# Optimization experiments

Measured on AMD Instinct MI355X. Metric: run time of the kernel, lower is better.

Reference implementation:

```python
import jax, jax.numpy as jnp
import numpy as np

B, T, K = 32, 8192, 16
EPS = 1e-7
LAM_FIRE, LAM_CANCEL, LAM_VALID, LAM_WRITE = 1.0, 1.0, 0.5, 0.5


def setup_inputs() -> dict:
    key = jax.random.key(0)
    ks = jax.random.split(key, 11)
    return {
        "trigger_hazard": jax.random.uniform(ks[0], (B, T, K), jnp.float32),
        "validity": jax.random.uniform(ks[1], (B, T, K), jnp.float32),
        "cancel_logits": jax.random.normal(ks[2], (B, T, K, 3), jnp.float32),
        "write_score": jax.random.normal(ks[3], (B, T, 1), jnp.float32),
        "live_mask": jax.random.randint(ks[4], (B, T, K), 0, 2).astype(bool),
        "contract_id": jax.random.randint(ks[5], (B, T, K), 0, 32),
        "oracle_fire": jax.random.randint(ks[6], (B, T, K), 0, 2).astype(jnp.float32),
        "oracle_cancel": jax.random.randint(ks[7], (B, T, K), 0, 4),
        "oracle_valid": jax.random.randint(ks[8], (B, T, K), 0, 2).astype(jnp.float32),
        "oracle_should_write": jax.random.randint(ks[9], (B, T, 1), 0, 2).astype(jnp.float32),
        "oracle_contract_id": jax.random.randint(ks[10], (B, T, K), 0, 32),
    }


def _masked_bce(p_raw, y, m):
    # Mirrors torch: BCE(clamp(p)*mask, y*mask), then *mask, sum / clamp(mask.sum(),1)
    n = jnp.maximum(m.sum(), 1.0)
    p = jnp.clip(p_raw, EPS, 1.0 - EPS) * m
    t = y * m
    # extra inner clip only guards masked entries (p==0), which are zeroed anyway
    bce = -(t * jnp.log(jnp.clip(p, EPS)) + (1.0 - t) * jnp.log(jnp.clip(1.0 - p, EPS)))
    return (bce * m).sum() / n


def _cancel_ce(logits, cancel_tgt, live_mask):
    has = ((cancel_tgt > 0) & live_mask).astype(jnp.float32)  # (B,T,K)
    n = has.sum()
    tgt = jnp.clip(cancel_tgt - 1, 0).astype(jnp.int32)
    logp = jax.nn.log_softmax(logits, axis=-1)  # (B,T,K,3)
    ce = -jnp.take_along_axis(logp, tgt[..., None], axis=-1)[..., 0]
    return jnp.where(n > 0, (ce * has).sum() / jnp.maximum(n, 1.0), 0.0)


def _bce_with_logits(x, y):
    return jnp.mean(jnp.maximum(x, 0.0) - x * y + jnp.log1p(jnp.exp(-jnp.abs(x))))


def reference(trigger_hazard, validity, cancel_logits, write_score, live_mask,
              contract_id, oracle_fire, oracle_cancel, oracle_valid,
              oracle_should_write, oracle_contract_id):
    # Vectorized align_oracle_to_model: broadcast compare + first-match argmax + gather
    match = (contract_id[..., :, None] == oracle_contract_id[..., None, :]) \
            & (contract_id != 0)[..., None]              # (B,T,Km,Ko)
    found = match.any(axis=-1)                           # (B,T,Km)
    idx = jnp.argmax(match, axis=-1)                     # first matching oracle slot

    def align_f(x):  # float tensors -> zeros where unmatched (torch out = zeros float)
        return jnp.where(found, jnp.take_along_axis(x, idx, axis=2), 0.0)

    fire_t = align_f(oracle_fire)
    valid_t = align_f(oracle_valid)
    cancel_t = jnp.where(found, jnp.take_along_axis(oracle_cancel, idx, axis=2), 0)

    m = live_mask.astype(jnp.float32)
    fire = LAM_FIRE * _masked_bce(trigger_hazard, fire_t, m)
    cancel = LAM_CANCEL * _cancel_ce(cancel_logits, cancel_t, live_mask)
    valid = LAM_VALID * _masked_bce(validity, valid_t, m)
    write = LAM_WRITE * _bce_with_logits(write_score, oracle_should_write)
    total = fire + cancel + valid + write
    return jnp.stack([fire, cancel, valid, write, total])
```

## Files before the change

kernel.cpp:

```cpp
#include <hip/hip_runtime.h>
#include <math.h>

#define EPS_F 1e-7f

constexpr int Bc = 32, Tc = 8192, Kc = 16;
constexpr int ROWS   = Bc * Tc;
constexpr int BLOCK  = 256;
constexpr int NITEM4 = ROWS * 4;
constexpr int NBLK   = NITEM4 / BLOCK;
constexpr int ROWS_PER_BLK = BLOCK / 4;

constexpr int R_OCID = 0 * 4096;
constexpr int R_OCAN = 1 * 4096;
constexpr int R_OFIR = 2 * 4096;
constexpr int R_OVAL = 3 * 4096;
constexpr int R_CID  = 4 * 4096;
constexpr int R_LIVE = 5 * 4096;
constexpr int R_TRIG = 6 * 4096;
constexpr int R_VALP = 7 * 4096;
constexpr int R_CLOG = 8 * 4096;
constexpr int R_WSC  = R_CLOG + 12288;
constexpr int R_OSW  = R_WSC + 256;
constexpr int SMEM_BYTES = R_OSW + 256;

typedef unsigned long long u64;

__device__ __forceinline__ u64 shflx64(u64 v, int m) {
  unsigned lo = __shfl_xor((unsigned)v, m, 64);
  unsigned hi = __shfl_xor((unsigned)(v >> 32), m, 64);
  return ((u64)hi << 32) | lo;
}

__device__ __forceinline__ void dma16(void* lds, const void* g) {
  __builtin_amdgcn_global_load_lds(
      (const __attribute__((address_space(1))) void*)g,
      (__attribute__((address_space(3))) void*)lds, 16, 0, 0);
}
__device__ __forceinline__ void dma4(void* lds, const void* g) {
  __builtin_amdgcn_global_load_lds(
      (const __attribute__((address_space(1))) void*)g,
      (__attribute__((address_space(3))) void*)lds, 4, 0, 0);
}

__global__ __launch_bounds__(BLOCK) void loss_main(
    const float* __restrict__ trig,
    const float* __restrict__ valp,
    const float* __restrict__ clog,
    const float* __restrict__ wscore,
    const int*   __restrict__ live,
    const int*   __restrict__ cid,
    const float* __restrict__ ofire,
    const int*   __restrict__ ocan,
    const float* __restrict__ ovalid,
    const float* __restrict__ oshw,
    const int*   __restrict__ ocid,
    float* __restrict__ part)
{
  __shared__ __align__(16) char smem[SMEM_BYTES];

  const int tid  = threadIdx.x;
  const int lane = tid & 63;
  const int w    = tid >> 6;
  const int t0   = blockIdx.x * BLOCK;
  const int gi   = t0 + w * 64 + lane;

  {
    char* sb = smem + w * 1024;
    const size_t o16 = (size_t)gi * 16;
    dma16(sb + R_OCID, (const char*)ocid  + o16);
    dma16(sb + R_OCAN, (const char*)ocan  + o16);
    dma16(sb + R_OFIR, (const char*)ofire + o16);
    dma16(sb + R_OVAL, (const char*)ovalid+ o16);
    dma16(sb + R_CID,  (const char*)cid   + o16);
    dma16(sb + R_LIVE, (const char*)live  + o16);
    dma16(sb + R_TRIG, (const char*)trig  + o16);
    dma16(sb + R_VALP, (const char*)valp  + o16);
    const char* gc = (const char*)clog + (size_t)(t0 + w * 64) * 48;
    char* sc = smem + R_CLOG + w * 3072;
    dma16(sc + 0,    gc + 0    + lane * 16);
    dma16(sc + 1024, gc + 1024 + lane * 16);
    dma16(sc + 2048, gc + 2048 + lane * 16);
    const int r0 = blockIdx.x * ROWS_PER_BLK;
    if (w == 0)      dma4(smem + R_WSC, (const char*)wscore + (size_t)(r0 + lane) * 4);
    else if (w == 1) dma4(smem + R_OSW, (const char*)oshw   + (size_t)(r0 + lane) * 4);
  }
  __syncthreads();

  const int4   oc = *(const int4*)  (smem + R_OCID + tid * 16);
  const int4   cc = *(const int4*)  (smem + R_OCAN + tid * 16);
  const float4 ff = *(const float4*)(smem + R_OFIR + tid * 16);
  const float4 vv = *(const float4*)(smem + R_OVAL + tid * 16);
  const int4   cd = *(const int4*)  (smem + R_CID  + tid * 16);
  const int4   lm = *(const int4*)  (smem + R_LIVE + tid * 16);
  const float4 ph = *(const float4*)(smem + R_TRIG + tid * 16);
  const float4 pq = *(const float4*)(smem + R_VALP + tid * 16);
  const float4 lA = *(const float4*)(smem + R_CLOG + tid * 48 + 0);
  const float4 lB = *(const float4*)(smem + R_CLOG + tid * 48 + 16);
  const float4 lC = *(const float4*)(smem + R_CLOG + tid * 48 + 32);
  const float  wx = *(const float*) (smem + R_WSC + (tid >> 2) * 4);
  const float  wy = *(const float*) (smem + R_OSW + (tid >> 2) * 4);

  u64 tblLo = 0ull, tblHi = 0ull, fndLo = 0ull, fndHi = 0ull;
  {
    const int   ocs[4] = {oc.x, oc.y, oc.z, oc.w};
    const int   ccs[4] = {cc.x, cc.y, cc.z, cc.w};
    const float ffs[4] = {ff.x, ff.y, ff.z, ff.w};
    const float vvs[4] = {vv.x, vv.y, vv.z, vv.w};
    #pragma unroll
    for (int j = 0; j < 4; ++j) {
      const unsigned c  = (unsigned)ocs[j] & 31u;
      const unsigned sh = (c & 15u) * 4u;
      const bool isLo   = c < 16u;
      const bool seen   = (((isLo ? fndLo : fndHi) >> sh) & 1ull) != 0ull;
      const unsigned nib = (unsigned)ffs[j] | ((unsigned)vvs[j] << 1) |
                           ((unsigned)ccs[j] << 2);
      const u64 add  = seen ? 0ull : ((u64)nib << sh);
      const u64 fadd = 0xFull << sh;
      tblLo |= isLo ? add : 0ull;
      tblHi |= isLo ? 0ull : add;
      fndLo |= isLo ? fadd : 0ull;
      fndHi |= isLo ? 0ull : fadd;
    }
  }

  #pragma unroll
  for (int m = 1; m <= 2; m <<= 1) {
    const u64 pTL = shflx64(tblLo, m);
    const u64 pTH = shflx64(tblHi, m);
    const u64 pFL = shflx64(fndLo, m);
    const u64 pFH = shflx64(fndHi, m);
    const bool iLow = (lane & m) == 0;
    const u64 loTL = iLow ? tblLo : pTL, hiTL = iLow ? pTL : tblLo;
    const u64 loTH = iLow ? tblHi : pTH, hiTH = iLow ? pTH : tblHi;
    const u64 loFL = iLow ? fndLo : pFL, hiFL = iLow ? pFL : fndLo;
    const u64 loFH = iLow ? fndHi : pFH, hiFH = iLow ? pFH : fndHi;
    tblLo = loTL | (hiTL & ~loFL);
    tblHi = loTH | (hiTH & ~loFH);
    fndLo = loFL | hiFL;
    fndHi = loFH | hiFH;
  }

  float s0 = 0.f, s1 = 0.f, s2 = 0.f, s3 = 0.f, s4 = 0.f;
  {
    const int   cds[4] = {cd.x, cd.y, cd.z, cd.w};
    const int   lms[4] = {lm.x, lm.y, lm.z, lm.w};
    const float phs[4] = {ph.x, ph.y, ph.z, ph.w};
    const float pqs[4] = {pq.x, pq.y, pq.z, pq.w};
    const float L0[4] = {lA.x, lA.w, lB.z, lC.y};
    const float L1[4] = {lA.y, lB.x, lB.w, lC.z};
    const float L2[4] = {lA.z, lB.y, lC.x, lC.w};
    #pragma unroll
    for (int j = 0; j < 4; ++j) {
      const unsigned c  = (unsigned)cds[j] & 31u;
      const unsigned sh = (c & 15u) * 4u;
      const bool isLo   = c < 16u;
      const bool fnd = (c != 0u) &&
                       ((((isLo ? fndLo : fndHi) >> sh) & 1ull) != 0ull);
      unsigned nib = (unsigned)(((isLo ? tblLo : tblHi) >> sh)) & 15u;
      nib = fnd ? nib : 0u;
      const float fire_t = (float)(nib & 1u);
      const float val_t  = (float)((nib >> 1) & 1u);
      const int   can_t  = (int)(nib >> 2);

      const float m = lms[j] ? 1.f : 0.f;

      const float p  = fminf(fmaxf(phs[j], EPS_F), 1.f - EPS_F);
      const float bf = -__logf((fire_t != 0.f) ? p : 1.f - p);
      const float q  = fminf(fmaxf(pqs[j], EPS_F), 1.f - EPS_F);
      const float bv = -__logf((val_t != 0.f) ? q : 1.f - q);

      const float has = (can_t > 0 && lms[j]) ? 1.f : 0.f;
      const int tgt = (can_t - 1) < 0 ? 0 : (can_t - 1);
      const float l0 = L0[j], l1 = L1[j], l2 = L2[j];
      const float mx  = fmaxf(l0, fmaxf(l1, l2));
      const float lse = mx + __logf(__expf(l0 - mx) + __expf(l1 - mx) +
                                    __expf(l2 - mx));
      const float lt  = (tgt == 0) ? l0 : ((tgt == 1) ? l1 : l2);

      s0 += bf * m;
      s1 += m;
      s2 += (lse - lt) * has;
      s3 += has;
      s4 += bv * m;
    }
  }

  float s5 = 0.f;
  if ((tid & 3) == 0) {
    s5 = fmaxf(wx, 0.f) - wx * wy + __logf(1.f + __expf(-fabsf(wx)));
  }

  float v[6] = {s0, s1, s2, s3, s4, s5};
  #pragma unroll
  for (int off = 32; off > 0; off >>= 1) {
    #pragma unroll
    for (int i = 0; i < 6; ++i) v[i] += __shfl_down(v[i], off, 64);
  }
  __shared__ float red[4][6];
  if (lane == 0) {
    #pragma unroll
    for (int i = 0; i < 6; ++i) red[w][i] = v[i];
  }
  __syncthreads();
  if (tid == 0) {
    #pragma unroll
    for (int i = 0; i < 6; ++i)
      part[blockIdx.x * 6 + i] = red[0][i] + red[1][i] + red[2][i] + red[3][i];
  }
}

__global__ __launch_bounds__(BLOCK) void loss_finalize(
    const float* __restrict__ part, float* __restrict__ out)
{
  double v[6] = {0, 0, 0, 0, 0, 0};
  for (int r = threadIdx.x; r < NBLK; r += BLOCK) {
    #pragma unroll
    for (int i = 0; i < 6; ++i) v[i] += (double)part[r * 6 + i];
  }
  #pragma unroll
  for (int off = 32; off > 0; off >>= 1) {
    #pragma unroll
    for (int i = 0; i < 6; ++i) v[i] += __shfl_down(v[i], off, 64);
  }
  __shared__ double red[4][6];
  const int w = threadIdx.x >> 6, lane = threadIdx.x & 63;
  if (lane == 0) {
    #pragma unroll
    for (int i = 0; i < 6; ++i) red[w][i] = v[i];
  }
  __syncthreads();
  if (threadIdx.x == 0) {
    double a[6];
    #pragma unroll
    for (int i = 0; i < 6; ++i) a[i] = red[0][i] + red[1][i] + red[2][i] + red[3][i];
    const double live_n = a[1] < 1.0 ? 1.0 : a[1];
    const double fire   = a[0] / live_n;
    const double cancel = (a[3] > 0.0) ? a[2] / (a[3] < 1.0 ? 1.0 : a[3])
                                       : 0.0;
    const double valid  = 0.5 * a[4] / live_n;
    const double wr     = 0.5 * a[5] / (double)ROWS;
    out[0] = (float)fire;
    out[1] = (float)cancel;
    out[2] = (float)valid;
    out[3] = (float)wr;
    out[4] = (float)(fire + cancel + valid + wr);
  }
}

extern "C" void kernel_launch(void* const* d_in, const int* in_sizes, int n_in,
                              void* d_out, int out_size, void* d_ws, size_t ws_size,
                              hipStream_t stream) {
  const float* trig   = (const float*)d_in[0];
  const float* valp   = (const float*)d_in[1];
  const float* clog   = (const float*)d_in[2];
  const float* wscore = (const float*)d_in[3];
  const int*   live   = (const int*)  d_in[4];
  const int*   cid    = (const int*)  d_in[5];
  const float* ofire  = (const float*)d_in[6];
  const int*   ocan   = (const int*)  d_in[7];
  const float* ovalid = (const float*)d_in[8];
  const float* oshw   = (const float*)d_in[9];
  const int*   ocid   = (const int*)  d_in[10];
  float* out  = (float*)d_out;
  float* part = (float*)d_ws;

  loss_main<<<NBLK, BLOCK, 0, stream>>>(trig, valp, clog, wscore, live, cid,
                                        ofire, ocan, ovalid, oshw, ocid, part);
  loss_finalize<<<1, BLOCK, 0, stream>>>(part, out);
}
```

Measured before the change: 208.5 us.

## Switch to persistent grid with double-buffered LDS DMA pipeline

Replaces the one-tile-per-block launch with a fixed grid of 768 persistent 128-thread blocks. Each block walks tiles in a grid-stride loop and double-buffers the global-to-LDS DMA loads, using vmcnt waits so the next tile's loads overlap the current tile's compute. This removes per-block launch and tail overhead, and the finalize kernel now reduces far fewer partials. The risks are lower memory-level parallelism per CU, manual waitcnt correctness with no barriers between waves, and clamped tile indices on the last iteration.

```diff
diff --git a/kernel.cpp b/kernel.cpp
--- a/kernel.cpp
+++ b/kernel.cpp
@@ -3,25 +3,28 @@
 
 #define EPS_F 1e-7f
 
-constexpr int Bc = 32, Tc = 8192, Kc = 16;
-constexpr int ROWS   = Bc * Tc;
-constexpr int BLOCK  = 256;
-constexpr int NITEM4 = ROWS * 4;
-constexpr int NBLK   = NITEM4 / BLOCK;
-constexpr int ROWS_PER_BLK = BLOCK / 4;
-
-constexpr int R_OCID = 0 * 4096;
-constexpr int R_OCAN = 1 * 4096;
-constexpr int R_OFIR = 2 * 4096;
-constexpr int R_OVAL = 3 * 4096;
-constexpr int R_CID  = 4 * 4096;
-constexpr int R_LIVE = 5 * 4096;
-constexpr int R_TRIG = 6 * 4096;
-constexpr int R_VALP = 7 * 4096;
-constexpr int R_CLOG = 8 * 4096;
-constexpr int R_WSC  = R_CLOG + 12288;
+constexpr int ROWS  = 32 * 8192;
+constexpr int BLOCK = 128;
+constexpr int TILE_ITEMS = 128;
+constexpr int NT    = (ROWS * 4) / TILE_ITEMS;
+constexpr int GRID  = 768;
+constexpr int KIT   = (NT + GRID - 1) / GRID;
+
+constexpr int R_OCID = 0 * 2048;
+constexpr int R_OCAN = 1 * 2048;
+constexpr int R_OFIR = 2 * 2048;
+constexpr int R_OVAL = 3 * 2048;
+constexpr int R_CID  = 4 * 2048;
+constexpr int R_LIVE = 5 * 2048;
+constexpr int R_TRIG = 6 * 2048;
+constexpr int R_VALP = 7 * 2048;
+constexpr int R_CLOG = 8 * 2048;
+constexpr int R_WSC  = R_CLOG + 6144;
 constexpr int R_OSW  = R_WSC + 256;
-constexpr int SMEM_BYTES = R_OSW + 256;
+constexpr int BUFSZ  = R_OSW + 256;
+
+#define WAIT_VM12 0x0F7C
+#define WAIT_VM0  0x0F70
 
 typedef unsigned long long u64;
 
@@ -56,16 +59,18 @@
     const int*   __restrict__ ocid,
     float* __restrict__ part)
 {
-  __shared__ __align__(16) char smem[SMEM_BYTES];
+  __shared__ __align__(16) char smem[2 * BUFSZ];
 
   const int tid  = threadIdx.x;
   const int lane = tid & 63;
   const int w    = tid >> 6;
-  const int t0   = blockIdx.x * BLOCK;
-  const int gi   = t0 + w * 64 + lane;
-
-  {
-    char* sb = smem + w * 1024;
+
+  float s0 = 0.f, s1 = 0.f, s2 = 0.f, s3 = 0.f, s4 = 0.f, s5 = 0.f;
+
+  auto stage = [&](int tileC, int bufIdx) {
+    char* buf = smem + bufIdx * BUFSZ;
+    char* sb  = buf + w * 1024;
+    const int gi = tileC * TILE_ITEMS + w * 64 + lane;
     const size_t o16 = (size_t)gi * 16;
     dma16(sb + R_OCID, (const char*)ocid  + o16);
     dma16(sb + R_OCAN, (const char*)ocan  + o16);
@@ -75,119 +80,131 @@
     dma16(sb + R_LIVE, (const char*)live  + o16);
     dma16(sb + R_TRIG, (const char*)trig  + o16);
     dma16(sb + R_VALP, (const char*)valp  + o16);
-    const char* gc = (const char*)clog + (size_t)(t0 + w * 64) * 48;
-    char* sc = smem + R_CLOG + w * 3072;
+    const char* gc = (const char*)clog + (size_t)(tileC * TILE_ITEMS + w * 64) * 48;
+    char* sc = buf + R_CLOG + w * 3072;
     dma16(sc + 0,    gc + 0    + lane * 16);
     dma16(sc + 1024, gc + 1024 + lane * 16);
     dma16(sc + 2048, gc + 2048 + lane * 16);
-    const int r0 = blockIdx.x * ROWS_PER_BLK;
-    if (w == 0)      dma4(smem + R_WSC, (const char*)wscore + (size_t)(r0 + lane) * 4);
-    else if (w == 1) dma4(smem + R_OSW, (const char*)oshw   + (size_t)(r0 + lane) * 4);
-  }
-  __syncthreads();
-
-  const int4   oc = *(const int4*)  (smem + R_OCID + tid * 16);
-  const int4   cc = *(const int4*)  (smem + R_OCAN + tid * 16);
-  const float4 ff = *(const float4*)(smem + R_OFIR + tid * 16);
-  const float4 vv = *(const float4*)(smem + R_OVAL + tid * 16);
-  const int4   cd = *(const int4*)  (smem + R_CID  + tid * 16);
-  const int4   lm = *(const int4*)  (smem + R_LIVE + tid * 16);
-  const float4 ph = *(const float4*)(smem + R_TRIG + tid * 16);
-  const float4 pq = *(const float4*)(smem + R_VALP + tid * 16);
-  const float4 lA = *(const float4*)(smem + R_CLOG + tid * 48 + 0);
-  const float4 lB = *(const float4*)(smem + R_CLOG + tid * 48 + 16);
-  const float4 lC = *(const float4*)(smem + R_CLOG + tid * 48 + 32);
-  const float  wx = *(const float*) (smem + R_WSC + (tid >> 2) * 4);
-  const float  wy = *(const float*) (smem + R_OSW + (tid >> 2) * 4);
-
-  u64 tblLo = 0ull, tblHi = 0ull, fndLo = 0ull, fndHi = 0ull;
-  {
-    const int   ocs[4] = {oc.x, oc.y, oc.z, oc.w};
-    const int   ccs[4] = {cc.x, cc.y, cc.z, cc.w};
-    const float ffs[4] = {ff.x, ff.y, ff.z, ff.w};
-    const float vvs[4] = {vv.x, vv.y, vv.z, vv.w};
-    #pragma unroll
-    for (int j = 0; j < 4; ++j) {
-      const unsigned c  = (unsigned)ocs[j] & 31u;
-      const unsigned sh = (c & 15u) * 4u;
-      const bool isLo   = c < 16u;
-      const bool seen   = (((isLo ? fndLo : fndHi) >> sh) & 1ull) != 0ull;
-      const unsigned nib = (unsigned)ffs[j] | ((unsigned)vvs[j] << 1) |
-                           ((unsigned)ccs[j] << 2);
-      const u64 add  = seen ? 0ull : ((u64)nib << sh);
-      const u64 fadd = 0xFull << sh;
-      tblLo |= isLo ? add : 0ull;
-      tblHi |= isLo ? 0ull : add;
-      fndLo |= isLo ? fadd : 0ull;
-      fndHi |= isLo ? 0ull : fadd;
-    }
-  }
-
-  #pragma unroll
-  for (int m = 1; m <= 2; m <<= 1) {
-    const u64 pTL = shflx64(tblLo, m);
-    const u64 pTH = shflx64(tblHi, m);
-    const u64 pFL = shflx64(fndLo, m);
-    const u64 pFH = shflx64(fndHi, m);
-    const bool iLow = (lane & m) == 0;
-    const u64 loTL = iLow ? tblLo : pTL, hiTL = iLow ? pTL : tblLo;
-    const u64 loTH = iLow ? tblHi : pTH, hiTH = iLow ? pTH : tblHi;
-    const u64 loFL = iLow ? fndLo : pFL, hiFL = iLow ? pFL : fndLo;
-    const u64 loFH = iLow ? fndHi : pFH, hiFH = iLow ? pFH : fndHi;
-    tblLo = loTL | (hiTL & ~loFL);
-    tblHi = loTH | (hiTH & ~loFH);
-    fndLo = loFL | hiFL;
-    fndHi = loFH | hiFH;
-  }
-
-  float s0 = 0.f, s1 = 0.f, s2 = 0.f, s3 = 0.f, s4 = 0.f;
-  {
-    const int   cds[4] = {cd.x, cd.y, cd.z, cd.w};
-    const int   lms[4] = {lm.x, lm.y, lm.z, lm.w};
-    const float phs[4] = {ph.x, ph.y, ph.z, ph.w};
-    const float pqs[4] = {pq.x, pq.y, pq.z, pq.w};
-    const float L0[4] = {lA.x, lA.w, lB.z, lC.y};
-    const float L1[4] = {lA.y, lB.x, lB.w, lC.z};
-    const float L2[4] = {lA.z, lB.y, lC.x, lC.w};
-    #pragma unroll
-    for (int j = 0; j < 4; ++j) {
-      const unsigned c  = (unsigned)cds[j] & 31u;
-      const unsigned sh = (c & 15u) * 4u;
-      const bool isLo   = c < 16u;
-      const bool fnd = (c != 0u) &&
-                       ((((isLo ? fndLo : fndHi) >> sh) & 1ull) != 0ull);
-      unsigned nib = (unsigned)(((isLo ? tblLo : tblHi) >> sh)) & 15u;
-      nib = fnd ? nib : 0u;
-      const float fire_t = (float)(nib & 1u);
-      const float val_t  = (float)((nib >> 1) & 1u);
-      const int   can_t  = (int)(nib >> 2);
-
-      const float m = lms[j] ? 1.f : 0.f;
-
-      const float p  = fminf(fmaxf(phs[j], EPS_F), 1.f - EPS_F);
-      const float bf = -__logf((fire_t != 0.f) ? p : 1.f - p);
-      const float q  = fminf(fmaxf(pqs[j], EPS_F), 1.f - EPS_F);
-      const float bv = -__logf((val_t != 0.f) ? q : 1.f - q);
-
-      const float has = (can_t > 0 && lms[j]) ? 1.f : 0.f;
-      const int tgt = (can_t - 1) < 0 ? 0 : (can_t - 1);
-      const float l0 = L0[j], l1 = L1[j], l2 = L2[j];
-      const float mx  = fmaxf(l0, fmaxf(l1, l2));
-      const float lse = mx + __logf(__expf(l0 - mx) + __expf(l1 - mx) +
-                                    __expf(l2 - mx));
-      const float lt  = (tgt == 0) ? l0 : ((tgt == 1) ? l1 : l2);
-
-      s0 += bf * m;
-      s1 += m;
-      s2 += (lse - lt) * has;
-      s3 += has;
-      s4 += bv * m;
-    }
-  }
-
-  float s5 = 0.f;
-  if ((tid & 3) == 0) {
-    s5 = fmaxf(wx, 0.f) - wx * wy + __logf(1.f + __expf(-fabsf(wx)));
+    const int row = min(tileC * 32 + lane, ROWS - 1);
+    if (w == 0) dma4(buf + R_WSC, (const char*)wscore + (size_t)row * 4);
+    else        dma4(buf + R_OSW, (const char*)oshw   + (size_t)row * 4);
+  };
+
+  auto compute = [&](int bufIdx) {
+    const char* buf = smem + bufIdx * BUFSZ;
+    const int4   oc = *(const int4*)  (buf + R_OCID + tid * 16);
+    const int4   cc = *(const int4*)  (buf + R_OCAN + tid * 16);
+    const float4 ff = *(const float4*)(buf + R_OFIR + tid * 16);
+    const float4 vv = *(const float4*)(buf + R_OVAL + tid * 16);
+    const int4   cd = *(const int4*)  (buf + R_CID  + tid * 16);
+    const int4   lm = *(const int4*)  (buf + R_LIVE + tid * 16);
+    const float4 ph = *(const float4*)(buf + R_TRIG + tid * 16);
+    const float4 pq = *(const float4*)(buf + R_VALP + tid * 16);
+    const float4 lA = *(const float4*)(buf + R_CLOG + tid * 48 + 0);
+    const float4 lB = *(const float4*)(buf + R_CLOG + tid * 48 + 16);
+    const float4 lC = *(const float4*)(buf + R_CLOG + tid * 48 + 32);
+    const float  wx = *(const float*) (buf + R_WSC + (tid >> 2) * 4);
+    const float  wy = *(const float*) (buf + R_OSW + (tid >> 2) * 4);
+
+    u64 tblLo = 0ull, tblHi = 0ull, fndLo = 0ull, fndHi = 0ull;
+    {
+      const int   ocs[4] = {oc.x, oc.y, oc.z, oc.w};
+      const int   ccs[4] = {cc.x, cc.y, cc.z, cc.w};
+      const float ffs[4] = {ff.x, ff.y, ff.z, ff.w};
+      const float vvs[4] = {vv.x, vv.y, vv.z, vv.w};
+      #pragma unroll
+      for (int j = 0; j < 4; ++j) {
+        const unsigned c  = (unsigned)ocs[j] & 31u;
+        const unsigned sh = (c & 15u) * 4u;
+        const bool isLo   = c < 16u;
+        const bool seen   = (((isLo ? fndLo : fndHi) >> sh) & 1ull) != 0ull;
+        const unsigned nib = (unsigned)ffs[j] | ((unsigned)vvs[j] << 1) |
+                             ((unsigned)ccs[j] << 2);
+        const u64 add  = seen ? 0ull : ((u64)nib << sh);
+        const u64 fadd = 0xFull << sh;
+        tblLo |= isLo ? add : 0ull;
+        tblHi |= isLo ? 0ull : add;
+        fndLo |= isLo ? fadd : 0ull;
+        fndHi |= isLo ? 0ull : fadd;
+      }
+    }
+    #pragma unroll
+    for (int m = 1; m <= 2; m <<= 1) {
+      const u64 pTL = shflx64(tblLo, m);
+      const u64 pTH = shflx64(tblHi, m);
+      const u64 pFL = shflx64(fndLo, m);
+      const u64 pFH = shflx64(fndHi, m);
+      const bool iLow = (lane & m) == 0;
+      const u64 loTL = iLow ? tblLo : pTL, hiTL = iLow ? pTL : tblLo;
+      const u64 loTH = iLow ? tblHi : pTH, hiTH = iLow ? pTH : tblHi;
+      const u64 loFL = iLow ? fndLo : pFL, hiFL = iLow ? pFL : fndLo;
+      const u64 loFH = iLow ? fndHi : pFH, hiFH = iLow ? pFH : fndHi;
+      tblLo = loTL | (hiTL & ~loFL);
+      tblHi = loTH | (hiTH & ~loFH);
+      fndLo = loFL | hiFL;
+      fndHi = loFH | hiFH;
+    }
+    {
+      const int   cds[4] = {cd.x, cd.y, cd.z, cd.w};
+      const int   lms[4] = {lm.x, lm.y, lm.z, lm.w};
+      const float phs[4] = {ph.x, ph.y, ph.z, ph.w};
+      const float pqs[4] = {pq.x, pq.y, pq.z, pq.w};
+      const float L0[4] = {lA.x, lA.w, lB.z, lC.y};
+      const float L1[4] = {lA.y, lB.x, lB.w, lC.z};
+      const float L2[4] = {lA.z, lB.y, lC.x, lC.w};
+      #pragma unroll
+      for (int j = 0; j < 4; ++j) {
+        const unsigned c  = (unsigned)cds[j] & 31u;
+        const unsigned sh = (c & 15u) * 4u;
+        const bool isLo   = c < 16u;
+        const bool fnd = (c != 0u) &&
+                         ((((isLo ? fndLo : fndHi) >> sh) & 1ull) != 0ull);
+        unsigned nib = (unsigned)(((isLo ? tblLo : tblHi) >> sh)) & 15u;
+        nib = fnd ? nib : 0u;
+        const float fire_t = (float)(nib & 1u);
+        const float val_t  = (float)((nib >> 1) & 1u);
+        const int   can_t  = (int)(nib >> 2);
+
+        const float m = lms[j] ? 1.f : 0.f;
+
+        const float p  = fminf(fmaxf(phs[j], EPS_F), 1.f - EPS_F);
+        const float bf = -__logf((fire_t != 0.f) ? p : 1.f - p);
+        const float q  = fminf(fmaxf(pqs[j], EPS_F), 1.f - EPS_F);
+        const float bv = -__logf((val_t != 0.f) ? q : 1.f - q);
+
+        const float has = (can_t > 0 && lms[j]) ? 1.f : 0.f;
+        const int tgt = (can_t - 1) < 0 ? 0 : (can_t - 1);
+        const float l0 = L0[j], l1 = L1[j], l2 = L2[j];
+        const float mx  = fmaxf(l0, fmaxf(l1, l2));
+        const float lse = mx + __logf(__expf(l0 - mx) + __expf(l1 - mx) +
+                                      __expf(l2 - mx));
+        const float lt  = (tgt == 0) ? l0 : ((tgt == 1) ? l1 : l2);
+
+        s0 += bf * m;
+        s1 += m;
+        s2 += (lse - lt) * has;
+        s3 += has;
+        s4 += bv * m;
+      }
+    }
+    if ((tid & 3) == 0) {
+      s5 += fmaxf(wx, 0.f) - wx * wy + __logf(1.f + __expf(-fabsf(wx)));
+    }
+  };
+
+  const int b = blockIdx.x;
+  auto tileOf = [&](int k) { return b + k * GRID; };
+  auto tileC  = [&](int k) { int t = tileOf(k); return t < NT ? t : NT - 1; };
+
+  stage(tileC(0), 0);
+  stage(tileC(1), 1);
+  for (int k = 0; k < KIT; ++k) {
+    if (k == KIT - 1) __builtin_amdgcn_s_waitcnt(WAIT_VM0);
+    else              __builtin_amdgcn_s_waitcnt(WAIT_VM12);
+    __builtin_amdgcn_sched_barrier(0);
+    if (tileOf(k) < NT) compute(k & 1);
+    __builtin_amdgcn_sched_barrier(0);
+    if (k + 2 < KIT) stage(tileC(k + 2), k & 1);
   }
 
   float v[6] = {s0, s1, s2, s3, s4, s5};
@@ -196,7 +213,7 @@
     #pragma unroll
     for (int i = 0; i < 6; ++i) v[i] += __shfl_down(v[i], off, 64);
   }
-  __shared__ float red[4][6];
+  __shared__ float red[2][6];
   if (lane == 0) {
     #pragma unroll
     for (int i = 0; i < 6; ++i) red[w][i] = v[i];
@@ -205,15 +222,15 @@
   if (tid == 0) {
     #pragma unroll
     for (int i = 0; i < 6; ++i)
-      part[blockIdx.x * 6 + i] = red[0][i] + red[1][i] + red[2][i] + red[3][i];
-  }
-}
-
-__global__ __launch_bounds__(BLOCK) void loss_finalize(
+      part[b * 6 + i] = red[0][i] + red[1][i];
+  }
+}
+
+__global__ __launch_bounds__(256) void loss_finalize(
     const float* __restrict__ part, float* __restrict__ out)
 {
   double v[6] = {0, 0, 0, 0, 0, 0};
-  for (int r = threadIdx.x; r < NBLK; r += BLOCK) {
+  for (int r = threadIdx.x; r < GRID; r += 256) {
     #pragma unroll
     for (int i = 0; i < 6; ++i) v[i] += (double)part[r * 6 + i];
   }
@@ -264,7 +281,7 @@
   float* out  = (float*)d_out;
   float* part = (float*)d_ws;
 
-  loss_main<<<NBLK, BLOCK, 0, stream>>>(trig, valp, clog, wscore, live, cid,
+  loss_main<<<GRID, BLOCK, 0, stream>>>(trig, valp, clog, wscore, live, cid,
                                         ofire, ocan, ovalid, oshw, ocid, part);
-  loss_finalize<<<1, BLOCK, 0, stream>>>(part, out);
-}
+  loss_finalize<<<1, 256, 0, stream>>>(part, out);
+}
```

Measured after the change: 213.1 us. 1.02x slower.
